# Performance work log

Measured on AMD Instinct MI355X. Metric: run time of the kernel, lower is better.

## Reference

```python
import jax, jax.numpy as jnp
import numpy as np
import math

ALPHA = 1.0  # surrogate-gradient sharpness, self.alpha() == 1.0

@jax.custom_vjp
def spike(x):
    # Heaviside forward (PiecewiseQuadratic.apply forward)
    return (x >= 0).astype(x.dtype)

def _spike_fwd(x):
    return spike(x), x

def _spike_bwd(x, g):
    # piecewise-quadratic surrogate: g'(x) = alpha - alpha^2*|x| for |x| < 1/alpha, else 0
    sg = jnp.where(jnp.abs(x) < 1.0 / ALPHA, -(ALPHA ** 2) * jnp.abs(x) + ALPHA, 0.0)
    return (g * sg.astype(x.dtype),)

spike.defvjp(_spike_fwd, _spike_bwd)


def setup_inputs() -> dict:
    key = jax.random.key(0)
    kx = jax.random.fold_in(key, 0)
    B, T, N = 64, 64, 8192
    x = jax.random.normal(kx, (B, T, N), dtype=jnp.float32)
    # parameters per __init__: tau=2.0 -> stored param log(1/(tau-1)) = 0.0
    tau_p = jnp.array([math.log(1.0 / (2.0 - 1.0))], dtype=jnp.float32)
    lamb = jnp.array([0.2], dtype=jnp.float32)
    th = jnp.array([1.0], dtype=jnp.float32)  # non-learnable
    return {"x": x, "tau_p": tau_p, "lamb": lamb, "th": th}


def reference(x, tau_p, lamb, th):
    sig = jax.nn.sigmoid(tau_p)  # scalar leak factor, shape [1]
    xt = jnp.swapaxes(x, 0, 1)   # [T, B, N] for scan over time

    def step(last, x_t):
        u = last * sig + x_t
        s = spike(u - th)
        new_last = (u + lamb * (u - last)) * (1.0 - s)  # momentum + hard reset
        return new_last, s

    last0 = jnp.zeros_like(x[:, 0])
    _, out = jax.lax.scan(step, last0, xt)  # out: [T, B, N]
    return jnp.swapaxes(out, 0, 1)         # [B, T, N]
```

## Files before the change

### kernel.cpp

```cpp
#include <hip/hip_runtime.h>


#define LIF_B 64
#define LIF_T 64
#define LIF_N 8192
#define NV4 (LIF_N / 4)
#define UN 4
#define NSTAGE (LIF_T / UN)

typedef float f4 __attribute__((ext_vector_type(4)));

#define LIF_STEP(LREG, COMP)                                                   \
    {                                                                          \
        float u = __fadd_rn(__fmul_rn(LREG, sig), v.COMP);                     \
        float s = (u >= th) ? 1.0f : 0.0f;                                     \
        LREG = __fmul_rn(__fadd_rn(u, __fmul_rn(lamb, __fsub_rn(u, LREG))),    \
                         __fsub_rn(1.0f, s));                                  \
        sv.COMP = s;                                                           \
    }

__global__ __launch_bounds__(256) void lif_fwd_kernel(
    const f4* __restrict__ x,
    const float* __restrict__ tau_p,
    const float* __restrict__ lamb_p,
    const float* __restrict__ th_p,
    f4* __restrict__ out)
{
    const int tid = blockIdx.x * blockDim.x + threadIdx.x;
    const int b   = tid >> 11;
    const int n4  = tid & (NV4 - 1);

    const float sig  = 1.0f / (1.0f + expf(-tau_p[0]));
    const float lamb = lamb_p[0];
    const float th   = th_p[0];

    float l0 = 0.0f, l1 = 0.0f, l2 = 0.0f, l3 = 0.0f;
    const size_t base = (size_t)b * LIF_T * NV4 + n4;

    f4 cur[UN], mid[UN], nxt[UN];

#pragma unroll
    for (int i = 0; i < UN; ++i)
        cur[i] = x[base + (size_t)i * NV4];
#pragma unroll
    for (int i = 0; i < UN; ++i)
        mid[i] = x[base + (size_t)(UN + i) * NV4];

#pragma unroll
    for (int k = 0; k < NSTAGE; ++k) {
        if (k + 2 < NSTAGE) {
#pragma unroll
            for (int i = 0; i < UN; ++i)
                nxt[i] = x[base + (size_t)((k + 2) * UN + i) * NV4];
        }

#pragma unroll
        for (int i = 0; i < UN; ++i) {
            f4 v = cur[i];
            f4 sv;
            LIF_STEP(l0, x)
            LIF_STEP(l1, y)
            LIF_STEP(l2, z)
            LIF_STEP(l3, w)
            __builtin_nontemporal_store(sv, &out[base + (size_t)(k * UN + i) * NV4]);
        }

#pragma unroll
        for (int i = 0; i < UN; ++i) {
            cur[i] = mid[i];
            mid[i] = nxt[i];
        }
    }
}

extern "C" void kernel_launch(void* const* d_in, const int* in_sizes, int n_in,
                              void* d_out, int out_size, void* d_ws, size_t ws_size,
                              hipStream_t stream) {
    (void)in_sizes; (void)n_in; (void)out_size; (void)d_ws; (void)ws_size;

    const f4*    x     = (const f4*)d_in[0];
    const float* tau_p = (const float*)d_in[1];
    const float* lamb  = (const float*)d_in[2];
    const float* th    = (const float*)d_in[3];
    f4*          out   = (f4*)d_out;

    const int total_threads = LIF_B * NV4;
    const int block = 256;
    const int grid  = total_threads / block;

    lif_fwd_kernel<<<grid, block, 0, stream>>>(x, tau_p, lamb, th, out);
}
```

Measured before the change: 245.1 us.

## Process two float4 columns per thread and halve grid size

```diff
diff --git a/kernel.cpp b/kernel.cpp
--- a/kernel.cpp
+++ b/kernel.cpp
@@ -10,14 +10,17 @@
 
 typedef float f4 __attribute__((ext_vector_type(4)));
 
-#define LIF_STEP(LREG, COMP)                                                   \
+#define LIF_COMP(ST, VV, SS, C)                                                \
     {                                                                          \
-        float u = __fadd_rn(__fmul_rn(LREG, sig), v.COMP);                     \
+        float u = __fadd_rn(__fmul_rn(ST.C, sig), VV.C);                       \
         float s = (u >= th) ? 1.0f : 0.0f;                                     \
-        LREG = __fmul_rn(__fadd_rn(u, __fmul_rn(lamb, __fsub_rn(u, LREG))),    \
+        ST.C = __fmul_rn(__fadd_rn(u, __fmul_rn(lamb, __fsub_rn(u, ST.C))),    \
                          __fsub_rn(1.0f, s));                                  \
-        sv.COMP = s;                                                           \
+        SS.C = s;                                                              \
     }
+#define LIF_F4(ST, VV, SS)                                                     \
+    LIF_COMP(ST, VV, SS, x) LIF_COMP(ST, VV, SS, y)                            \
+    LIF_COMP(ST, VV, SS, z) LIF_COMP(ST, VV, SS, w)
 
 __global__ __launch_bounds__(256) void lif_fwd_kernel(
     const f4* __restrict__ x,
@@ -26,49 +29,54 @@
     const float* __restrict__ th_p,
     f4* __restrict__ out)
 {
-    const int tid = blockIdx.x * blockDim.x + threadIdx.x;
-    const int b   = tid >> 11;
-    const int n4  = tid & (NV4 - 1);
+    const int w  = threadIdx.x >> 6;
+    const int l  = threadIdx.x & 63;
+    const int b  = blockIdx.x >> 2;
+    const int c0 = ((blockIdx.x & 3) << 9) | (w << 7) | l;
 
     const float sig  = 1.0f / (1.0f + expf(-tau_p[0]));
     const float lamb = lamb_p[0];
     const float th   = th_p[0];
 
-    float l0 = 0.0f, l1 = 0.0f, l2 = 0.0f, l3 = 0.0f;
-    const size_t base = (size_t)b * LIF_T * NV4 + n4;
+    const size_t base = (size_t)b * (LIF_T * NV4) + c0;
 
-    f4 cur[UN], mid[UN], nxt[UN];
+    f4 stA = {0.0f, 0.0f, 0.0f, 0.0f};
+    f4 stB = {0.0f, 0.0f, 0.0f, 0.0f};
+
+    f4 cur[UN][2], nxt[UN][2];
 
 #pragma unroll
-    for (int i = 0; i < UN; ++i)
-        cur[i] = x[base + (size_t)i * NV4];
-#pragma unroll
-    for (int i = 0; i < UN; ++i)
-        mid[i] = x[base + (size_t)(UN + i) * NV4];
+    for (int i = 0; i < UN; ++i) {
+        const size_t o = base + (size_t)i * NV4;
+        cur[i][0] = x[o];
+        cur[i][1] = x[o + 64];
+    }
 
 #pragma unroll
     for (int k = 0; k < NSTAGE; ++k) {
-        if (k + 2 < NSTAGE) {
+        if (k + 1 < NSTAGE) {
 #pragma unroll
-            for (int i = 0; i < UN; ++i)
-                nxt[i] = x[base + (size_t)((k + 2) * UN + i) * NV4];
+            for (int i = 0; i < UN; ++i) {
+                const size_t o = base + (size_t)((k + 1) * UN + i) * NV4;
+                nxt[i][0] = x[o];
+                nxt[i][1] = x[o + 64];
+            }
         }
 
 #pragma unroll
         for (int i = 0; i < UN; ++i) {
-            f4 v = cur[i];
-            f4 sv;
-            LIF_STEP(l0, x)
-            LIF_STEP(l1, y)
-            LIF_STEP(l2, z)
-            LIF_STEP(l3, w)
-            __builtin_nontemporal_store(sv, &out[base + (size_t)(k * UN + i) * NV4]);
+            const size_t o = base + (size_t)(k * UN + i) * NV4;
+            f4 s0, s1;
+            LIF_F4(stA, cur[i][0], s0)
+            LIF_F4(stB, cur[i][1], s1)
+            __builtin_nontemporal_store(s0, &out[o]);
+            __builtin_nontemporal_store(s1, &out[o + 64]);
         }
 
 #pragma unroll
         for (int i = 0; i < UN; ++i) {
-            cur[i] = mid[i];
-            mid[i] = nxt[i];
+            cur[i][0] = nxt[i][0];
+            cur[i][1] = nxt[i][1];
         }
     }
 }
@@ -84,9 +92,7 @@
     const float* th    = (const float*)d_in[3];
     f4*          out   = (f4*)d_out;
 
-    const int total_threads = LIF_B * NV4;
     const int block = 256;
-    const int grid  = total_threads / block;
-
+    const int grid  = 256;
     lif_fwd_kernel<<<grid, block, 0, stream>>>(x, tau_p, lamb, th, out);
 }
```

After: 235.9 us. -3.8%, faster.
